# Optimization experiments

Hardware: AMD Instinct MI355X
Metric: run time of the kernel (lower is better)

Reference implementation:

```python
import jax, jax.numpy as jnp
import numpy as np

B, T, D_MODEL, D_STATE = 8, 2048, 1024, 256


def setup_inputs() -> dict:
    key = jax.random.key(0)
    ks = jax.random.split(key, 11)
    def lecun(k, shape):
        fan_in = shape[0]
        return jax.random.normal(k, shape, jnp.float32) / jnp.sqrt(jnp.float32(fan_in))
    return {
        "x": jax.random.normal(ks[0], (B, T, D_MODEL), jnp.float32),
        "W_in": lecun(ks[1], (D_MODEL, D_STATE)),
        "b_in": jnp.zeros((D_STATE,), jnp.float32),
        "W_gate": lecun(ks[2], (D_MODEL, D_MODEL)),
        "b_gate": jnp.zeros((D_MODEL,), jnp.float32),
        "A": lecun(ks[3], (D_STATE, D_STATE)),
        "Bm": lecun(ks[4], (D_STATE, D_STATE)),
        "C": lecun(ks[5], (D_MODEL, D_STATE)),
        "D": lecun(ks[6], (D_MODEL, D_STATE)),
        "W_out": lecun(ks[7], (D_MODEL, D_MODEL)),
        "b_out": jnp.zeros((D_MODEL,), jnp.float32),
    }


def reference(x, W_in, b_in, W_gate, b_gate, A, Bm, C, D, W_out, b_out):
    b, t, d_model = x.shape
    d_state = A.shape[0]
    u = x @ W_in + b_in                      # [B,T,d_state]
    g = jax.nn.sigmoid(x @ W_gate + b_gate)  # [B,T,d_model]

    u_seq = jnp.swapaxes(u, 0, 1)  # [T,B,d_state]
    g_seq = jnp.swapaxes(g, 0, 1)  # [T,B,d_model]
    x_seq = jnp.swapaxes(x, 0, 1)  # [T,B,d_model]

    def step(h_prev, inputs):
        u_t, g_t, x_t = inputs
        h_t = jnp.tanh(h_prev @ A + u_t @ Bm)            # [B,d_state]
        y_t = h_t @ C.T + u_t @ D.T                      # [B,d_model]
        y_t = g_t * y_t + (1.0 - g_t) * x_t
        return h_t, y_t

    h0 = jnp.zeros((b, d_state), x.dtype)
    _, ys = jax.lax.scan(step, h0, xs=(u_seq, g_seq, x_seq))
    ys = jnp.swapaxes(ys, 0, 1)  # [B,T,d_model]
    return ys @ W_out + b_out + x
```

## Files before the change

kernel.cpp:

```cpp
#include <hip/hip_runtime.h>
#include <math.h>


enum { E_NONE = 0, E_BIASBF = 1, E_SIGBF = 2, E_GATE = 3, E_BIASRES = 4,
       E_CVTBF = 5, E_BIASF32 = 6 };

typedef __attribute__((ext_vector_type(8))) short bf16x8;
typedef __attribute__((ext_vector_type(4))) float f32x4;

static __device__ inline unsigned short f2bf(float f) {
    unsigned u = __builtin_bit_cast(unsigned, f);
    unsigned r = (u + 0x7fff + ((u >> 16) & 1)) >> 16;
    return (unsigned short)r;
}
static __device__ inline unsigned pack2(float a, float b) {
    return (unsigned)f2bf(a) | ((unsigned)f2bf(b) << 16);
}
static __device__ inline float bflo(unsigned u) {
    return __builtin_bit_cast(float, u << 16);
}
static __device__ inline float bfhi(unsigned u) {
    return __builtin_bit_cast(float, u & 0xffff0000u);
}
static __device__ inline float tanh_fast(float x) {
    float e = __builtin_amdgcn_exp2f(x * 2.8853900817779268f);
    float t = __builtin_amdgcn_rcpf(e + 1.0f);
    return fmaf(-2.0f, t, 1.0f);
}

static __device__ __forceinline__ void cvt_body(
    const float* __restrict__ in, unsigned short* __restrict__ out, int i, int n8)
{
    if (i >= n8) return;
    float4 a = ((const float4*)in)[i * 2];
    float4 b = ((const float4*)in)[i * 2 + 1];
    uint4 o;
    o.x = pack2(a.x, a.y); o.y = pack2(a.z, a.w);
    o.z = pack2(b.x, b.y); o.w = pack2(b.z, b.w);
    ((uint4*)out)[i] = o;
}

static __device__ __forceinline__ void transpose_tile(
    bool act, unsigned char* LdsB, int bxi, int byi, int t2,
    const float* __restrict__ in, unsigned short* __restrict__ out, int R, int C)
{
    float* tile = (float*)LdsB;
    const int bx = bxi * 32, by = byi * 32;
    const int tx = t2 & 31, ty = t2 >> 5;
    if (act) {
#pragma unroll
        for (int i = 0; i < 32; i += 8)
            tile[(ty + i) * 33 + tx] = in[(size_t)(by + ty + i) * C + bx + tx];
    }
    __syncthreads();
    if (act) {
#pragma unroll
        for (int i = 0; i < 32; i += 8)
            out[(size_t)(bx + ty + i) * R + by + tx] = f2bf(tile[tx * 33 + ty + i]);
    }
}

__global__ __launch_bounds__(256) void prep_all(
    const float* __restrict__ x, unsigned short* __restrict__ xbf,
    const float* __restrict__ W_in, unsigned short* __restrict__ Winbf,
    const float* __restrict__ Dm, unsigned short* __restrict__ Dbf,
    const float* __restrict__ Bm, unsigned short* __restrict__ BmT,
    const float* __restrict__ W_gate, unsigned short* __restrict__ WgT,
    const float* __restrict__ b_in, float* __restrict__ b2, float* __restrict__ bD)
{
    __shared__ __align__(16) unsigned char Lds[32 * 33 * 4];
    const unsigned bid = blockIdx.x;
    const int tid = threadIdx.x;
    if (bid < 8192) {
        cvt_body(x, xbf, bid * 256 + tid, 16384 * 1024 / 8);
    } else if (bid < 8320) {
        cvt_body(W_in, Winbf, (bid - 8192) * 256 + tid, 1024 * 256 / 8);
    } else if (bid < 8448) {
        cvt_body(Dm, Dbf, (bid - 8320) * 256 + tid, 1024 * 256 / 8);
    } else if (bid < 8512) {
        const int t = bid - 8448;
        transpose_tile(true, Lds, t & 7, t >> 3, tid, Bm, BmT, 256, 256);
    } else if (bid < 9536) {
        const int t = bid - 8512;
        transpose_tile(true, Lds, t & 31, t >> 5, tid, W_gate, WgT, 1024, 1024);
    } else if (bid == 9536) {
        float s = 0.f;
        for (int k = 0; k < 256; ++k) s = fmaf(b_in[k], Bm[k * 256 + tid], s);
        b2[tid] = s;
    } else {
        const int n = (bid - 9537) * 256 + tid;
        float s = 0.f;
        for (int k = 0; k < 256; ++k) s = fmaf(b_in[k], Dm[n * 256 + k], s);
        bD[n] = s;
    }
}

template <int EPI>
static __device__ __forceinline__ void gemm_tile(
    bool act, unsigned char* Lds, int bx, int by, int tid,
    const unsigned short* __restrict__ Ag,
    const unsigned short* __restrict__ Bg,
    const float* __restrict__ bias, const float* __restrict__ res,
    const float* __restrict__ acc_src, const unsigned short* __restrict__ g8,
    void* Cg, int M, int N, int K)
{
    const int w = (tid >> 6) & 3, l = tid & 63;
    const int r = l & 15, g = l >> 4;
    const int m0 = by * 128, n0 = bx * 128;

    const unsigned char* agp[4];
    const unsigned char* bgp[4];
#pragma unroll
    for (int j = 0; j < 4; ++j) {
        const int c = w * 256 + j * 64 + l;
        const int row = c >> 3;
        const unsigned offp = ((unsigned)(c & 7) * 16u) ^ ((unsigned)(row & 7) * 16u);
        agp[j] = (const unsigned char*)Ag + ((size_t)(m0 + row) * K) * 2 + offp;
        bgp[j] = (const unsigned char*)Bg + ((size_t)(n0 + row) * K) * 2 + offp;
    }

#define GSTAGE(BUF)                                                           \
    {                                                                         \
      _Pragma("unroll")                                                       \
      for (int j = 0; j < 4; ++j) {                                           \
        __builtin_amdgcn_global_load_lds(                                     \
            (const __attribute__((address_space(1))) unsigned*)(agp[j]),      \
            (__attribute__((address_space(3))) unsigned*)(Lds + (BUF) * 32768 + w * 4096 + j * 1024), \
            16, 0, 0);                                                        \
        __builtin_amdgcn_global_load_lds(                                     \
            (const __attribute__((address_space(1))) unsigned*)(bgp[j]),      \
            (__attribute__((address_space(3))) unsigned*)(Lds + (BUF) * 32768 + 16384 + w * 4096 + j * 1024), \
            16, 0, 0);                                                        \
        agp[j] += 128; bgp[j] += 128;                                         \
      }                                                                       \
    }

    f32x4 acc[2][8];
#pragma unroll
    for (int mt = 0; mt < 2; ++mt)
#pragma unroll
        for (int nt = 0; nt < 8; ++nt) acc[mt][nt] = (f32x4){0.f, 0.f, 0.f, 0.f};

    const int nk = K >> 6;
    if (act) GSTAGE(0)
    __syncthreads();
    for (int t = 0; t < nk; ++t) {
        const int buf = t & 1;
        if (act) {
            if (t + 1 < nk) GSTAGE(buf ^ 1)
            bf16x8 af[2][2], bfr[8][2];
#pragma unroll
            for (int s = 0; s < 2; ++s) {
#pragma unroll
                for (int mt = 0; mt < 2; ++mt) {
                    const int row = w * 32 + mt * 16 + r;
                    af[mt][s] = *(const bf16x8*)(Lds + buf * 32768 + row * 128 +
                        ((s * 64 + 16 * g) ^ (16 * (row & 7))));
                }
#pragma unroll
                for (int nt = 0; nt < 8; ++nt) {
                    const int row = nt * 16 + r;
                    bfr[nt][s] = *(const bf16x8*)(Lds + buf * 32768 + 16384 + row * 128 +
                        ((s * 64 + 16 * g) ^ (16 * (row & 7))));
                }
            }
#pragma unroll
            for (int s = 0; s < 2; ++s)
#pragma unroll
                for (int mt = 0; mt < 2; ++mt)
#pragma unroll
                    for (int nt = 0; nt < 8; ++nt)
                        acc[mt][nt] = __builtin_amdgcn_mfma_f32_16x16x32_bf16(
                            af[mt][s], bfr[nt][s], acc[mt][nt], 0, 0, 0);
        }
        __syncthreads();
    }
#undef GSTAGE

    if (act) {
#pragma unroll
        for (int mt = 0; mt < 2; ++mt)
#pragma unroll
            for (int nt = 0; nt < 8; ++nt) {
                const int n = n0 + nt * 16 + r;
                float bv = 0.f;
                if (EPI == E_BIASBF || EPI == E_SIGBF || EPI == E_BIASRES ||
                    EPI == E_BIASF32) bv = bias[n];
#pragma unroll
                for (int q = 0; q < 4; ++q) {
                    const int m = m0 + w * 32 + mt * 16 + g * 4 + q;
                    const size_t idx = (size_t)m * N + n;
                    float v = acc[mt][nt][q] + bv;
                    if (EPI == E_SIGBF) v = 1.f / (1.f + expf(-v));
                    if (EPI == E_BIASRES) v += res[idx];
                    if (EPI == E_GATE) {
                        v += acc_src[idx];
                        const float gg = bflo((unsigned)g8[idx]);
                        v = gg * v + (1.f - gg) * res[idx];
                    }
                    if (EPI == E_BIASBF || EPI == E_SIGBF || EPI == E_CVTBF ||
                        EPI == E_GATE)
                        ((unsigned short*)Cg)[idx] = f2bf(v);
                    else
                        ((float*)Cg)[idx] = v;
                }
            }
    }
}

template <int EPI>
__global__ __launch_bounds__(256) void gemm_mfma(
    const unsigned short* __restrict__ Ag, const unsigned short* __restrict__ Bg,
    const float* __restrict__ bias, const float* __restrict__ res,
    const float* __restrict__ acc_src, const unsigned short* __restrict__ g8,
    void* Cg, int M, int N, int K)
{
    __shared__ __align__(16) unsigned char Lds[65536];
    gemm_tile<EPI>(true, Lds, blockIdx.x, blockIdx.y, threadIdx.x,
                   Ag, Bg, bias, res, acc_src, g8, Cg, M, N, K);
}

static __device__ __forceinline__ void scan_body(
    unsigned char* LDSM, int tid,
    const float* __restrict__ Amat, const unsigned short* __restrict__ u2bf,
    unsigned short* __restrict__ hbf)
{
    constexpr int T = 2048;
    constexpr int NCH = T / 8;
    unsigned char* Hb = LDSM;
    unsigned char* Ub = LDSM + 65536;

    const int w = tid >> 6, l = tid & 63;
    const int r = l & 15, g = l >> 4, r8 = r & 7;
    const bool hi = (r & 8) != 0;
    const int m0 = w * 32;

    ((unsigned*)Hb)[tid] = 0u;
    ((unsigned*)Hb)[tid + 512] = 0u;

    bf16x8 af[2][8];
#pragma unroll
    for (int mt = 0; mt < 2; ++mt) {
        const int m = m0 + mt * 16 + r;
#pragma unroll
        for (int kt = 0; kt < 8; ++kt) {
            unsigned wd[4];
#pragma unroll
            for (int jw = 0; jw < 4; ++jw) {
                const int k = kt * 32 + g * 8 + jw * 2;
                wd[jw] = pack2(Amat[(size_t)k * 256 + m],
                               Amat[(size_t)(k + 1) * 256 + m]);
            }
            af[mt][kt] = __builtin_bit_cast(bf16x8, *(uint4*)wd);
        }
    }

    unsigned ubase[2], woff[2];
#pragma unroll
    for (int mt = 0; mt < 2; ++mt) {
        const int s0 = m0 + mt * 16 + g * 4;
        const int s = s0 + (hi ? 2 : 0);
        ubase[mt] = (unsigned)(r8 * 512 + (((s >> 3) ^ r8) * 16) + (s & 7) * 2);
        woff[mt] = (unsigned)((((s0 >> 5) * 32 + ((s0 >> 3) & 3) * 8 + r8) * 16)
                              + ((s0 & 7) + (hi ? 2 : 0)) * 2);
    }
    const unsigned rbase = (unsigned)((g * 8 + r8) * 16);

    int sg_i[4], sg_b[4], sg_kg[4];
#pragma unroll
    for (int j = 0; j < 4; ++j) {
        const int d = j * 512 + tid;
        sg_i[j] = d >> 8;
        sg_b[j] = (d >> 5) & 7;
        sg_kg[j] = (d & 31) ^ sg_b[j];
    }

#pragma unroll
    for (int c0 = 0; c0 < 2; ++c0)
#pragma unroll
        for (int j = 0; j < 4; ++j) {
            const size_t srcb = ((size_t)(sg_b[j] * T + c0 * 8 + sg_i[j]) * 512)
                              + (unsigned)(sg_kg[j] * 16);
            __builtin_amdgcn_global_load_lds(
                (const __attribute__((address_space(1))) unsigned*)(
                    (const unsigned char*)u2bf + srcb),
                (__attribute__((address_space(3))) unsigned*)(
                    Ub + c0 * 32768 + (j * 512 + tid) * 16), 16, 0, 0);
        }
    asm volatile("s_waitcnt vmcnt(0) lgkmcnt(0)" ::: "memory");
    __builtin_amdgcn_sched_barrier(0);
    __builtin_amdgcn_s_barrier();
    __builtin_amdgcn_sched_barrier(0);

#define SCAN_STEP(I)                                                          \
  {                                                                           \
    const unsigned sr = ((unsigned)(t0 + (I)) & 15u) * 4096u;                 \
    const unsigned sw = ((unsigned)(t0 + (I) + 1) & 15u) * 4096u;             \
    bf16x8 hf[8];                                                             \
    _Pragma("unroll")                                                         \
    for (int kt = 0; kt < 8; ++kt)                                            \
      hf[kt] = *(const bf16x8*)(Hb + sr + rbase + (unsigned)(kt * 512));      \
    unsigned uv[2];                                                           \
    _Pragma("unroll")                                                         \
    for (int mt = 0; mt < 2; ++mt)                                            \
      uv[mt] = *(const unsigned*)(Uc + (unsigned)(I) * 4096u + ubase[mt]);    \
    f32x4 p0[2], p1[2];                                                       \
    _Pragma("unroll")                                                         \
    for (int mt = 0; mt < 2; ++mt) {                                          \
      p0[mt] = (f32x4){0.f, 0.f, 0.f, 0.f};                                   \
      p1[mt] = (f32x4){0.f, 0.f, 0.f, 0.f};                                   \
    }                                                                         \
    _Pragma("unroll")                                                         \
    for (int kt = 0; kt < 4; ++kt) {                                          \
      _Pragma("unroll")                                                       \
      for (int mt = 0; mt < 2; ++mt) {                                        \
        p0[mt] = __builtin_amdgcn_mfma_f32_16x16x32_bf16(af[mt][kt], hf[kt],  \
                                                         p0[mt], 0, 0, 0);    \
        p1[mt] = __builtin_amdgcn_mfma_f32_16x16x32_bf16(                     \
            af[mt][kt + 4], hf[kt + 4], p1[mt], 0, 0, 0);                     \
      }                                                                       \
    }                                                                         \
    _Pragma("unroll")                                                         \
    for (int mt = 0; mt < 2; ++mt) {                                          \
      const float slo = hi ? (p0[mt][2] + p1[mt][2]) : (p0[mt][0] + p1[mt][0]);\
      const float shi = hi ? (p0[mt][3] + p1[mt][3]) : (p0[mt][1] + p1[mt][1]);\
      const float h0 = tanh_fast(slo + bflo(uv[mt]));                         \
      const float h1 = tanh_fast(shi + bfhi(uv[mt]));                         \
      unsigned pk;                                                            \
      asm("v_cvt_pk_bf16_f32 %0, %1, %2" : "=v"(pk) : "v"(h0), "v"(h1));      \
      *(unsigned*)(Hb + sw + woff[mt]) = pk;                                  \
    }                                                                         \
    asm volatile("s_waitcnt lgkmcnt(0)" ::: "memory");                        \
    __builtin_amdgcn_sched_barrier(0);                                        \
    __builtin_amdgcn_s_barrier();                                             \
    __builtin_amdgcn_sched_barrier(0);                                        \
  }

    for (int chunk = 0; chunk < NCH; ++chunk) {
        const int t0 = chunk * 8;
        const unsigned char* Uc = Ub + ((unsigned)(chunk & 1) << 15);

        SCAN_STEP(0)
        SCAN_STEP(1)
        SCAN_STEP(2)
        SCAN_STEP(3)
        SCAN_STEP(4)
        SCAN_STEP(5)
        SCAN_STEP(6)
        SCAN_STEP(7)

        {
#pragma unroll
            for (int j = 0; j < 4; ++j) {
                const int p = j * 512 + tid;
                const int di = p >> 8, wp = p & 255;
                const int kt_ = wp >> 5, sl_ = wp & 31;
                const unsigned slot = (unsigned)((t0 + 1 + di) & 15) * 4096u;
                uint4 dat = *(const uint4*)(Hb + slot + (unsigned)wp * 16u);
                const size_t off = ((size_t)((sl_ & 7) * T + t0 + di) * 256 +
                                    kt_ * 32 + (sl_ >> 3) * 8);
                *(uint4*)(hbf + off) = dat;
            }
            if (chunk + 2 < NCH) {
                const unsigned nb = (unsigned)(chunk & 1) << 15;
#pragma unroll
                for (int j = 0; j < 4; ++j) {
                    const size_t srcb =
                        ((size_t)(sg_b[j] * T + t0 + 16 + sg_i[j]) * 512)
                        + (unsigned)(sg_kg[j] * 16);
                    __builtin_amdgcn_global_load_lds(
                        (const __attribute__((address_space(1))) unsigned*)(
                            (const unsigned char*)u2bf + srcb),
                        (__attribute__((address_space(3))) unsigned*)(
                            Ub + nb + (j * 512 + tid) * 16), 16, 0, 0);
                }
                asm volatile("s_waitcnt vmcnt(8) lgkmcnt(0)" ::: "memory");
            } else {
                asm volatile("s_waitcnt vmcnt(4) lgkmcnt(0)" ::: "memory");
            }
            __builtin_amdgcn_sched_barrier(0);
            __builtin_amdgcn_s_barrier();
            __builtin_amdgcn_sched_barrier(0);
        }
    }
#undef SCAN_STEP
}

__global__ __launch_bounds__(512, 1) void fused_scan(
    const float* __restrict__ Amat, const unsigned short* __restrict__ u2bf,
    unsigned short* __restrict__ hbf,
    const unsigned short* __restrict__ xbf, const unsigned short* __restrict__ WgT,
    const float* __restrict__ b_gate, unsigned short* __restrict__ gbf,
    const unsigned short* __restrict__ WDT, const float* __restrict__ bD,
    float* __restrict__ big,
    const float* __restrict__ W_out, unsigned short* __restrict__ WoT,
    const float* __restrict__ Cm, unsigned short* __restrict__ Cbf,
    int M, int DM, int DS)
{
    __shared__ __align__(16) unsigned char LDSM[131072];
    const int tid = threadIdx.x;
    const unsigned bid = blockIdx.x;

    if (bid == 0) {
        scan_body(LDSM, tid, Amat, u2bf, hbf);
        return;
    }
    const bool act = tid < 256;
    const int t2 = tid & 255;
    if (bid <= 1024) {
        const int t = bid - 1;
        gemm_tile<E_SIGBF>(act, LDSM, t & 7, t >> 3, t2, xbf, WgT, b_gate,
                           nullptr, nullptr, nullptr, gbf, M, DM, DM);
    } else if (bid <= 2048) {
        const int t = bid - 1025;
        gemm_tile<E_BIASF32>(act, LDSM, t & 7, t >> 3, t2, xbf, WDT, bD,
                             nullptr, nullptr, nullptr, big, M, DM, DM);
    } else if (bid <= 3072) {
        const int t = bid - 2049;
        transpose_tile(act, LDSM, t & 31, t >> 5, t2, W_out, WoT, DM, DM);
    } else {
        const int t = bid - 3073;
        if (act) cvt_body(Cm, Cbf, t * 256 + t2, DM * DS / 8);
    }
}

extern "C" void kernel_launch(void* const* d_in, const int* in_sizes, int n_in,
                              void* d_out, int out_size, void* d_ws, size_t ws_size,
                              hipStream_t stream)
{
    const float* x      = (const float*)d_in[0];
    const float* W_in   = (const float*)d_in[1];
    const float* b_in   = (const float*)d_in[2];
    const float* W_gate = (const float*)d_in[3];
    const float* b_gate = (const float*)d_in[4];
    const float* Amat   = (const float*)d_in[5];
    const float* Bm     = (const float*)d_in[6];
    const float* Cm     = (const float*)d_in[7];
    const float* Dm     = (const float*)d_in[8];
    const float* W_out  = (const float*)d_in[9];
    const float* b_out  = (const float*)d_in[10];

    const int T = 2048, DM = 1024, DS = 256;
    const int M = 8 * T;
    const size_t MB = 1024 * 1024;
    char* ws = (char*)d_ws;

    unsigned short* xbf   = (unsigned short*)(ws);
    unsigned short* ysbf  = xbf;
    unsigned short* Winbf = (unsigned short*)(ws + 32 * MB);
    unsigned short* Dbf   = (unsigned short*)(ws + 33 * MB);
    unsigned short* W2T   = (unsigned short*)(ws + 34 * MB);
    unsigned short* WDT   = (unsigned short*)(ws + 35 * MB);
    float*          b2    = (float*)(ws + 38 * MB);
    float*          bD    = (float*)(ws + 38 * MB + 65536);
    unsigned short* u2    = (unsigned short*)(ws + 40 * MB);
    unsigned short* h     = (unsigned short*)(ws + 56 * MB);
    unsigned short* BmT   = (unsigned short*)(ws + 64 * MB);
    unsigned short* WgT   = (unsigned short*)(ws + 65 * MB);
    unsigned short* WoT   = (unsigned short*)(ws + 67 * MB);
    unsigned short* Cbf   = (unsigned short*)(ws + 69 * MB);
    float*          big   = (float*)(ws + 70 * MB);
    unsigned short* gbf   = (unsigned short*)(ws + 134 * MB);

    prep_all<<<9541, 256, 0, stream>>>(x, xbf, W_in, Winbf, Dm, Dbf, Bm, BmT,
                                       W_gate, WgT, b_in, b2, bD);

    gemm_mfma<E_CVTBF><<<dim3(DM / 128, DS / 128), 256, 0, stream>>>(
        BmT, Winbf, nullptr, nullptr, nullptr, nullptr, W2T, DS, DM, DS);
    gemm_mfma<E_CVTBF><<<dim3(DM / 128, DM / 128), 256, 0, stream>>>(
        Dbf, Winbf, nullptr, nullptr, nullptr, nullptr, WDT, DM, DM, DS);

    gemm_mfma<E_BIASBF><<<dim3(DS / 128, M / 128), 256, 0, stream>>>(
        xbf, W2T, b2, nullptr, nullptr, nullptr, u2, M, DS, DM);

    fused_scan<<<3201, 512, 0, stream>>>(
        Amat, u2, h, xbf, WgT, b_gate, gbf, WDT, bD, big, W_out, WoT, Cm, Cbf,
        M, DM, DS);

    gemm_mfma<E_GATE><<<dim3(DM / 128, M / 128), 256, 0, stream>>>(
        h, Cbf, nullptr, x, big, gbf, ysbf, M, DM, DS);
    gemm_mfma<E_BIASRES><<<dim3(DM / 128, M / 128), 256, 0, stream>>>(
        ysbf, WoT, b_out, x, nullptr, nullptr, (float*)d_out, M, DM, DM);
}
```

Baseline: 1.453 ms.

## Fuse output GEMMs into scan kernel with progress-flag dataflow overlap

Moves the W_out transpose and C conversion into the prep kernel and folds the gated C-projection and output GEMMs into the persistent scan kernel. Blocks spin on global atomic counters (scan progress every 16 chunks, gate/WD completion, per-row-tile completion) so downstream tiles start while the sequential scan is still running. This hides the tail GEMMs behind the latency-bound scan. It relies on the waiting blocks not starving the blocks they wait for, which risks deadlock if scheduling order differs, and it adds spin-wait and fence overhead.

```diff
diff --git a/kernel.cpp b/kernel.cpp
--- a/kernel.cpp
+++ b/kernel.cpp
@@ -26,6 +26,14 @@
     float e = __builtin_amdgcn_exp2f(x * 2.8853900817779268f);
     float t = __builtin_amdgcn_rcpf(e + 1.0f);
     return fmaf(-2.0f, t, 1.0f);
+}
+
+static __device__ __forceinline__ void wait_ge(unsigned* p, unsigned tgt, int tid) {
+    if (tid == 0) {
+        while (atomicAdd(p, 0u) < tgt) __builtin_amdgcn_s_sleep(2);
+        __threadfence();
+    }
+    __syncthreads();
 }
 
 static __device__ __forceinline__ void cvt_body(
@@ -66,6 +74,8 @@
     const float* __restrict__ Dm, unsigned short* __restrict__ Dbf,
     const float* __restrict__ Bm, unsigned short* __restrict__ BmT,
     const float* __restrict__ W_gate, unsigned short* __restrict__ WgT,
+    const float* __restrict__ W_out, unsigned short* __restrict__ WoT,
+    const float* __restrict__ Cm, unsigned short* __restrict__ Cbf,
     const float* __restrict__ b_in, float* __restrict__ b2, float* __restrict__ bD)
 {
     __shared__ __align__(16) unsigned char Lds[32 * 33 * 4];
@@ -83,12 +93,17 @@
     } else if (bid < 9536) {
         const int t = bid - 8512;
         transpose_tile(true, Lds, t & 31, t >> 5, tid, W_gate, WgT, 1024, 1024);
-    } else if (bid == 9536) {
+    } else if (bid < 10560) {
+        const int t = bid - 9536;
+        transpose_tile(true, Lds, t & 31, t >> 5, tid, W_out, WoT, 1024, 1024);
+    } else if (bid < 10688) {
+        cvt_body(Cm, Cbf, (bid - 10560) * 256 + tid, 1024 * 256 / 8);
+    } else if (bid == 10688) {
         float s = 0.f;
         for (int k = 0; k < 256; ++k) s = fmaf(b_in[k], Bm[k * 256 + tid], s);
         b2[tid] = s;
     } else {
-        const int n = (bid - 9537) * 256 + tid;
+        const int n = (bid - 10689) * 256 + tid;
         float s = 0.f;
         for (int k = 0; k < 256; ++k) s = fmaf(b_in[k], Dm[n * 256 + k], s);
         bD[n] = s;
@@ -223,7 +238,7 @@
 static __device__ __forceinline__ void scan_body(
     unsigned char* LDSM, int tid,
     const float* __restrict__ Amat, const unsigned short* __restrict__ u2bf,
-    unsigned short* __restrict__ hbf)
+    unsigned short* __restrict__ hbf, unsigned* __restrict__ scan_prog)
 {
     constexpr int T = 2048;
     constexpr int NCH = T / 8;
@@ -376,11 +391,15 @@
                 }
                 asm volatile("s_waitcnt vmcnt(8) lgkmcnt(0)" ::: "memory");
             } else {
-                asm volatile("s_waitcnt vmcnt(4) lgkmcnt(0)" ::: "memory");
+                asm volatile("s_waitcnt vmcnt(0) lgkmcnt(0)" ::: "memory");
             }
             __builtin_amdgcn_sched_barrier(0);
             __builtin_amdgcn_s_barrier();
             __builtin_amdgcn_sched_barrier(0);
+            if ((chunk & 15) == 15 && tid == 0) {
+                __threadfence();
+                atomicAdd(scan_prog, 1u);
+            }
         }
     }
 #undef SCAN_STEP
@@ -393,16 +412,22 @@
     const float* __restrict__ b_gate, unsigned short* __restrict__ gbf,
     const unsigned short* __restrict__ WDT, const float* __restrict__ bD,
     float* __restrict__ big,
-    const float* __restrict__ W_out, unsigned short* __restrict__ WoT,
-    const float* __restrict__ Cm, unsigned short* __restrict__ Cbf,
+    const unsigned short* __restrict__ Cbf, unsigned short* __restrict__ ysbf,
+    const unsigned short* __restrict__ WoT, const float* __restrict__ b_out,
+    const float* __restrict__ x, float* __restrict__ outp,
+    unsigned* __restrict__ flags,
     int M, int DM, int DS)
 {
     __shared__ __align__(16) unsigned char LDSM[131072];
     const int tid = threadIdx.x;
     const unsigned bid = blockIdx.x;
+    unsigned* scan_prog = flags + 0;
+    unsigned* gate_done = flags + 1;
+    unsigned* wd_done   = flags + 2;
+    unsigned* cg_done   = flags + 16;
 
     if (bid == 0) {
-        scan_body(LDSM, tid, Amat, u2bf, hbf);
+        scan_body(LDSM, tid, Amat, u2bf, hbf, scan_prog);
         return;
     }
     const bool act = tid < 256;
@@ -411,16 +436,39 @@
         const int t = bid - 1;
         gemm_tile<E_SIGBF>(act, LDSM, t & 7, t >> 3, t2, xbf, WgT, b_gate,
                            nullptr, nullptr, nullptr, gbf, M, DM, DM);
+        asm volatile("s_waitcnt vmcnt(0)" ::: "memory");
+        __syncthreads();
+        if (tid == 0) { __threadfence(); atomicAdd(gate_done, 1u); }
     } else if (bid <= 2048) {
         const int t = bid - 1025;
         gemm_tile<E_BIASF32>(act, LDSM, t & 7, t >> 3, t2, xbf, WDT, bD,
                              nullptr, nullptr, nullptr, big, M, DM, DM);
-    } else if (bid <= 3072) {
+        asm volatile("s_waitcnt vmcnt(0)" ::: "memory");
+        __syncthreads();
+        if (tid == 0) { __threadfence(); atomicAdd(wd_done, 1u); }
+    } else {
         const int t = bid - 2049;
-        transpose_tile(act, LDSM, t & 31, t >> 5, t2, W_out, WoT, DM, DM);
-    } else {
-        const int t = bid - 3073;
-        if (act) cvt_body(Cm, Cbf, t * 256 + t2, DM * DS / 8);
+        const int tg = t >> 7;
+        const int r128 = t & 127;
+        if (r128 < 64) {
+            const int b = r128 >> 3, bx = r128 & 7;
+            const int by = b * 16 + tg;
+            wait_ge(gate_done, 1024, tid);
+            wait_ge(wd_done, 1024, tid);
+            wait_ge(scan_prog, (unsigned)(tg + 1), tid);
+            gemm_tile<E_GATE>(act, LDSM, bx, by, t2, hbf, Cbf, nullptr, x,
+                              big, gbf, ysbf, M, DM, DS);
+            asm volatile("s_waitcnt vmcnt(0)" ::: "memory");
+            __syncthreads();
+            if (tid == 0) { __threadfence(); atomicAdd(&cg_done[by], 1u); }
+        } else {
+            const int o = r128 - 64;
+            const int b = o >> 3, bx = o & 7;
+            const int by = b * 16 + tg;
+            wait_ge(&cg_done[by], 8, tid);
+            gemm_tile<E_BIASRES>(act, LDSM, bx, by, t2, ysbf, WoT, b_out, x,
+                                 nullptr, nullptr, outp, M, DM, DM);
+        }
     }
 }
 
@@ -453,6 +501,7 @@
     unsigned short* WDT   = (unsigned short*)(ws + 35 * MB);
     float*          b2    = (float*)(ws + 38 * MB);
     float*          bD    = (float*)(ws + 38 * MB + 65536);
+    unsigned*       flags = (unsigned*)(ws + 39 * MB);
     unsigned short* u2    = (unsigned short*)(ws + 40 * MB);
     unsigned short* h     = (unsigned short*)(ws + 56 * MB);
     unsigned short* BmT   = (unsigned short*)(ws + 64 * MB);
@@ -462,8 +511,11 @@
     float*          big   = (float*)(ws + 70 * MB);
     unsigned short* gbf   = (unsigned short*)(ws + 134 * MB);
 
-    prep_all<<<9541, 256, 0, stream>>>(x, xbf, W_in, Winbf, Dm, Dbf, Bm, BmT,
-                                       W_gate, WgT, b_in, b2, bD);
+    hipMemsetAsync(flags, 0, 4096, stream);
+
+    prep_all<<<10693, 256, 0, stream>>>(x, xbf, W_in, Winbf, Dm, Dbf, Bm, BmT,
+                                        W_gate, WgT, W_out, WoT, Cm, Cbf,
+                                        b_in, b2, bD);
 
     gemm_mfma<E_CVTBF><<<dim3(DM / 128, DS / 128), 256, 0, stream>>>(
         BmT, Winbf, nullptr, nullptr, nullptr, nullptr, W2T, DS, DM, DS);
@@ -473,12 +525,7 @@
     gemm_mfma<E_BIASBF><<<dim3(DS / 128, M / 128), 256, 0, stream>>>(
         xbf, W2T, b2, nullptr, nullptr, nullptr, u2, M, DS, DM);
 
-    fused_scan<<<3201, 512, 0, stream>>>(
-        Amat, u2, h, xbf, WgT, b_gate, gbf, WDT, bD, big, W_out, WoT, Cm, Cbf,
-        M, DM, DS);
-
-    gemm_mfma<E_GATE><<<dim3(DM / 128, M / 128), 256, 0, stream>>>(
-        h, Cbf, nullptr, x, big, gbf, ysbf, M, DM, DS);
-    gemm_mfma<E_BIASRES><<<dim3(DM / 128, M / 128), 256, 0, stream>>>(
-        ysbf, WoT, b_out, x, nullptr, nullptr, (float*)d_out, M, DM, DM);
-}
+    fused_scan<<<4097, 512, 0, stream>>>(
+        Amat, u2, h, xbf, WgT, b_gate, gbf, WDT, bD, big,
+        Cbf, ysbf, WoT, b_out, x, (float*)d_out, flags, M, DM, DS);
+}
```

Result: no change. 1.441 ms, median of 2 (-0.8%).
